# Optimization experiments

Measured on AMD Instinct MI355X. Metric: run time of the kernel, lower is better.

## Reference

```python
import jax, jax.numpy as jnp
import numpy as np

N_NODES = 50000
N_EDGES = 1600000
IN_DIM = 256
HID = 128
HEADS = 1
N_CLASSES = 40
NEG_SLOPE = 0.2


def gat_conv(x, W, a_src, a_dst, b, src, dst, concat):
    """PyG GATConv (eval mode). x: [N, F_in]; W: [H*C, F_in]; a_*: [H, C]; b: bias."""
    N = x.shape[0]
    H, C = a_src.shape
    h = (x @ W.T).reshape(N, H, C)                       # [N, H, C]
    alpha_src = jnp.sum(h * a_src, axis=-1)              # [N, H]
    alpha_dst = jnp.sum(h * a_dst, axis=-1)              # [N, H]
    e = jax.nn.leaky_relu(alpha_src[src] + alpha_dst[dst], NEG_SLOPE)  # [E, H]
    # scatter-softmax over incoming edges of each destination node
    m = jax.ops.segment_max(e, dst, num_segments=N)
    m = jnp.where(jnp.isfinite(m), m, 0.0)               # nodes with no in-edges
    ex = jnp.exp(e - m[dst])
    denom = jax.ops.segment_sum(ex, dst, num_segments=N)
    alpha = ex / jnp.maximum(denom[dst], 1e-16)          # [E, H]
    out = jax.ops.segment_sum(h[src] * alpha[..., None], dst, num_segments=N)  # [N, H, C]
    out = out.reshape(N, H * C) if concat else out.mean(axis=1)
    return out + b


def setup_inputs() -> dict:
    key = jax.random.key(0)
    ks = jax.random.split(key, 10)
    glorot = lambda k, shape: jax.random.normal(k, shape, jnp.float32) * np.sqrt(2.0 / (shape[0] + shape[-1]))
    x = jax.random.normal(ks[0], (N_NODES, IN_DIM), jnp.float32)
    edge_index = jax.random.randint(ks[1], (2, N_EDGES), 0, N_NODES, jnp.int64)
    # layer 0: in=IN_DIM -> hidden, heads=HEADS, concat=True
    W0 = glorot(ks[2], (HEADS * HID, IN_DIM))
    a_src0 = glorot(ks[3], (HEADS, HID))
    a_dst0 = glorot(ks[4], (HEADS, HID))
    b0 = jnp.zeros((HEADS * HID,), jnp.float32)
    # layer 1: in=hidden*heads -> n_classes, concat=False
    W1 = glorot(ks[5], (HEADS * N_CLASSES, HEADS * HID))
    a_src1 = glorot(ks[6], (HEADS, N_CLASSES))
    a_dst1 = glorot(ks[7], (HEADS, N_CLASSES))
    b1 = jnp.zeros((N_CLASSES,), jnp.float32)
    return {"x": x, "edge_index": edge_index,
            "W0": W0, "a_src0": a_src0, "a_dst0": a_dst0, "b0": b0,
            "W1": W1, "a_src1": a_src1, "a_dst1": a_dst1, "b1": b1}


def reference(x, edge_index, W0, a_src0, a_dst0, b0, W1, a_src1, a_dst1, b1):
    N = x.shape[0]
    # PyG GATConv default add_self_loops=True (each layer adds them transiently)
    loop = jnp.arange(N, dtype=edge_index.dtype)
    src = jnp.concatenate([edge_index[0], loop])
    dst = jnp.concatenate([edge_index[1], loop])
    h = gat_conv(x, W0, a_src0, a_dst0, b0, src, dst, concat=True)
    h = jax.nn.relu(h)  # dropout is identity in eval mode
    out = gat_conv(h, W1, a_src1, a_dst1, b1, src, dst, concat=False)
    return out
```

## Files before the change

### kernel.cpp

```cpp
#include <hip/hip_runtime.h>
#include <hip/hip_bf16.h>

#define N_NODES 50000
#define N_EDGES 1600000
#define ET (N_EDGES + N_NODES)
#define IN_DIM 256
#define HID 128
#define NCLS 40
#define NEG 0.2f
#define NBUCK 391
#define CHUNK 4096
#define CAP 5120
#define SCATB ((ET + CHUNK - 1) / CHUNK)
#define GEMMB ((N_NODES + 63) / 64)

typedef short bf16x8 __attribute__((ext_vector_type(8)));
typedef float f32x4  __attribute__((ext_vector_type(4)));

__device__ __forceinline__ unsigned pk2(float a, float b) {
    __hip_bfloat16 ha = __float2bfloat16(a), hb = __float2bfloat16(b);
    unsigned short ua = *(unsigned short*)&ha, ub = *(unsigned short*)&hb;
    return (unsigned)ua | ((unsigned)ub << 16);
}
__device__ __forceinline__ float blo(unsigned u) { return __uint_as_float(u << 16); }
__device__ __forceinline__ float bhi(unsigned u) { return __uint_as_float(u & 0xffff0000u); }

__global__ void k_init(int* __restrict__ cursor) {
    int i = blockIdx.x * 256 + threadIdx.x;
    if (i < NBUCK) cursor[i] = i * CAP;
}

__global__ __launch_bounds__(256) void k_fused(
    const int* __restrict__ ei, int* __restrict__ cursor, unsigned int* __restrict__ buf,
    const float* __restrict__ x, const float* __restrict__ W0,
    const float* __restrict__ a_s, const float* __restrict__ a_d,
    unsigned short* __restrict__ h0b, float* __restrict__ as0, float* __restrict__ ad0) {
    __shared__ unsigned pool[6912];
    int t = threadIdx.x;

    if (blockIdx.x < SCATB) {
        int* sd    = (int*)pool;
        int* hist  = (int*)pool + 4096;
        int* wbase = (int*)pool + 4487;
        for (int i = t; i < NBUCK; i += 256) hist[i] = 0;
        __syncthreads();
        int base = blockIdx.x * CHUNK;
        #pragma unroll
        for (int j = 0; j < 16; ++j) {
            int i = base + j * 256 + t;
            int d = -1;
            if (i < ET) d = (i < N_EDGES) ? ei[N_EDGES + i] : (i - N_EDGES);
            sd[j * 256 + t] = d;
            if (d >= 0) atomicAdd(&hist[d >> 7], 1);
        }
        __syncthreads();
        for (int i = t; i < NBUCK; i += 256) {
            int h = hist[i];
            wbase[i] = h ? atomicAdd(&cursor[i], h) : 0;
            hist[i] = 0;
        }
        __syncthreads();
        #pragma unroll
        for (int j = 0; j < 16; ++j) {
            int i = base + j * 256 + t;
            int d = sd[j * 256 + t];
            if (d >= 0) {
                int s_ = (i < N_EDGES) ? ei[i] : d;
                int b = d >> 7;
                int off = atomicAdd(&hist[b], 1);
                buf[wbase[b] + off] = ((unsigned)(d & 127) << 16) | (unsigned)s_;
            }
        }
        return;
    }

    unsigned* sA = pool;
    unsigned* sB = pool + 2304;
    int n0 = (blockIdx.x - SCATB) * 64;
    int w = t >> 6, lane = t & 63;
    int rw = lane & 15, q = lane >> 4;
    f32x4 acc[8];
    #pragma unroll
    for (int n = 0; n < 8; ++n) acc[n] = (f32x4){0.f, 0.f, 0.f, 0.f};

    for (int kc = 0; kc < IN_DIM; kc += 64) {
        #pragma unroll
        for (int i = 0; i < 4; ++i) {
            int f = i * 256 + t;
            int r = f >> 4, fq = f & 15;
            float4 v = make_float4(0.f, 0.f, 0.f, 0.f);
            if (n0 + r < N_NODES)
                v = *(const float4*)&x[(size_t)(n0 + r) * IN_DIM + kc + fq * 4];
            *(uint2*)&sA[r * 36 + fq * 2] = make_uint2(pk2(v.x, v.y), pk2(v.z, v.w));
        }
        #pragma unroll
        for (int i = 0; i < 8; ++i) {
            int f = i * 256 + t;
            int c = f >> 4, fq = f & 15;
            float4 v = *(const float4*)&W0[(size_t)c * IN_DIM + kc + fq * 4];
            *(uint2*)&sB[c * 36 + fq * 2] = make_uint2(pk2(v.x, v.y), pk2(v.z, v.w));
        }
        __syncthreads();
        #pragma unroll
        for (int ks = 0; ks < 2; ++ks) {
            bf16x8 af = *(const bf16x8*)((const unsigned short*)sA + (16 * w + rw) * 72 + ks * 32 + q * 8);
            #pragma unroll
            for (int n = 0; n < 8; ++n) {
                bf16x8 bfr = *(const bf16x8*)((const unsigned short*)sB + (n * 16 + rw) * 72 + ks * 32 + q * 8);
                acc[n] = __builtin_amdgcn_mfma_f32_16x16x32_bf16(af, bfr, acc[n], 0, 0, 0);
            }
        }
        __syncthreads();
    }

    float asv[8], adv[8];
    #pragma unroll
    for (int n = 0; n < 8; ++n) { asv[n] = a_s[n * 16 + rw]; adv[n] = a_d[n * 16 + rw]; }
    float ps[4] = {0.f, 0.f, 0.f, 0.f}, pd[4] = {0.f, 0.f, 0.f, 0.f};
    #pragma unroll
    for (int n = 0; n < 8; ++n)
        #pragma unroll
        for (int reg = 0; reg < 4; ++reg) {
            float vv = acc[n][reg];
            ps[reg] += vv * asv[n];
            pd[reg] += vv * adv[n];
        }
    #pragma unroll
    for (int reg = 0; reg < 4; ++reg) {
        int node = n0 + 16 * w + q * 4 + reg;
        if (node < N_NODES) {
            #pragma unroll
            for (int n = 0; n < 8; ++n) {
                __hip_bfloat16 hb = __float2bfloat16(acc[n][reg]);
                h0b[(size_t)node * HID + n * 16 + rw] = *(unsigned short*)&hb;
            }
        }
    }
    #pragma unroll
    for (int reg = 0; reg < 4; ++reg)
        #pragma unroll
        for (int off = 1; off < 16; off <<= 1) {
            ps[reg] += __shfl_xor(ps[reg], off);
            pd[reg] += __shfl_xor(pd[reg], off);
        }
    if (rw == 0) {
        #pragma unroll
        for (int reg = 0; reg < 4; ++reg) {
            int node = n0 + 16 * w + q * 4 + reg;
            if (node < N_NODES) { as0[node] = ps[reg]; ad0[node] = pd[reg]; }
        }
    }
}

__global__ __launch_bounds__(256) void k_bucket_build(const unsigned int* __restrict__ buf,
                                                      const int* __restrict__ cursor,
                                                      int* __restrict__ rp, int* __restrict__ re,
                                                      int* __restrict__ csr) {
    __shared__ int cnt[128], rpl[128], cur[128];
    int b = blockIdx.x;
    int t = threadIdx.x;
    int lo = b * CAP, hi = cursor[b];
    if (t < 128) cnt[t] = 0;
    __syncthreads();
    for (int i = lo + t; i < hi; i += 256) atomicAdd(&cnt[buf[i] >> 16], 1);
    __syncthreads();
    if (t == 0) {
        int run = 0;
        #pragma unroll
        for (int l = 0; l < 128; ++l) { rpl[l] = run; run += cnt[l]; }
    }
    __syncthreads();
    if (t < 128) {
        int node = b * 128 + t;
        if (node < N_NODES) { rp[node] = lo + rpl[t]; re[node] = lo + rpl[t] + cnt[t]; }
        cur[t] = 0;
    }
    __syncthreads();
    for (int i = lo + t; i < hi; i += 256) {
        unsigned v = buf[i];
        int dl = v >> 16;
        int off = atomicAdd(&cur[dl], 1);
        csr[lo + rpl[dl] + off] = (int)(v & 0xffffu);
    }
}

__global__ __launch_bounds__(256) void k_agg0(
    const uint4* __restrict__ h0q, const float* __restrict__ as, const float* __restrict__ ad,
    const int* __restrict__ rp, const int* __restrict__ re, const int* __restrict__ csr,
    const float* __restrict__ bias, unsigned short* __restrict__ actb) {
    __shared__ float sw_[4][64];
    __shared__ int   ss_[4][64];
    int wid = threadIdx.x >> 6, lane = threadIdx.x & 63;
    int q = lane >> 4, ql = lane & 15;
    int node = blockIdx.x * 4 + wid;
    int start = rp[node], end = re[node];
    float ad_n = ad[node];
    float a0 = 0.f, a1 = 0.f, a2 = 0.f, a3 = 0.f;
    float a4 = 0.f, a5 = 0.f, a6 = 0.f, a7 = 0.f, den = 0.f;
    for (int base = start; base < end; base += 64) {
        int mm = end - base; if (mm > 64) mm = 64;
        int s_l = 0; float w_l = 0.f;
        if (lane < mm) {
            s_l = csr[base + lane];
            float e = as[s_l] + ad_n;
            e = (e > 0.f) ? e : NEG * e;
            w_l = __expf(e);
            den += w_l;
        }
        ss_[wid][lane] = s_l;
        sw_[wid][lane] = w_l;
        for (int jj = 0; jj < mm; jj += 16) {
            int i0 = jj + q, i1 = i0 + 4, i2 = i0 + 8, i3 = i0 + 12;
            int   s0 = ss_[wid][i0], s1 = ss_[wid][i1], s2 = ss_[wid][i2], s3 = ss_[wid][i3];
            float w0 = sw_[wid][i0], w1 = sw_[wid][i1], w2 = sw_[wid][i2], w3 = sw_[wid][i3];
            uint4 u0 = h0q[(size_t)s0 * 16 + ql];
            uint4 u1 = h0q[(size_t)s1 * 16 + ql];
            uint4 u2 = h0q[(size_t)s2 * 16 + ql];
            uint4 u3 = h0q[(size_t)s3 * 16 + ql];
            a0 += w0 * blo(u0.x) + w1 * blo(u1.x) + w2 * blo(u2.x) + w3 * blo(u3.x);
            a1 += w0 * bhi(u0.x) + w1 * bhi(u1.x) + w2 * bhi(u2.x) + w3 * bhi(u3.x);
            a2 += w0 * blo(u0.y) + w1 * blo(u1.y) + w2 * blo(u2.y) + w3 * blo(u3.y);
            a3 += w0 * bhi(u0.y) + w1 * bhi(u1.y) + w2 * bhi(u2.y) + w3 * bhi(u3.y);
            a4 += w0 * blo(u0.z) + w1 * blo(u1.z) + w2 * blo(u2.z) + w3 * blo(u3.z);
            a5 += w0 * bhi(u0.z) + w1 * bhi(u1.z) + w2 * bhi(u2.z) + w3 * bhi(u3.z);
            a6 += w0 * blo(u0.w) + w1 * blo(u1.w) + w2 * blo(u2.w) + w3 * blo(u3.w);
            a7 += w0 * bhi(u0.w) + w1 * bhi(u1.w) + w2 * bhi(u2.w) + w3 * bhi(u3.w);
        }
    }
    #pragma unroll
    for (int off = 32; off; off >>= 1) den += __shfl_xor(den, off);
    a0 += __shfl_xor(a0, 16); a0 += __shfl_xor(a0, 32);
    a1 += __shfl_xor(a1, 16); a1 += __shfl_xor(a1, 32);
    a2 += __shfl_xor(a2, 16); a2 += __shfl_xor(a2, 32);
    a3 += __shfl_xor(a3, 16); a3 += __shfl_xor(a3, 32);
    a4 += __shfl_xor(a4, 16); a4 += __shfl_xor(a4, 32);
    a5 += __shfl_xor(a5, 16); a5 += __shfl_xor(a5, 32);
    a6 += __shfl_xor(a6, 16); a6 += __shfl_xor(a6, 32);
    a7 += __shfl_xor(a7, 16); a7 += __shfl_xor(a7, 32);
    if (lane < 16) {
        float inv = 1.f / fmaxf(den, 1e-16f);
        float4 b0v = *(const float4*)&bias[ql * 8];
        float4 b1v = *(const float4*)&bias[ql * 8 + 4];
        float r0 = fmaxf(a0 * inv + b0v.x, 0.f);
        float r1 = fmaxf(a1 * inv + b0v.y, 0.f);
        float r2 = fmaxf(a2 * inv + b0v.z, 0.f);
        float r3 = fmaxf(a3 * inv + b0v.w, 0.f);
        float r4 = fmaxf(a4 * inv + b1v.x, 0.f);
        float r5 = fmaxf(a5 * inv + b1v.y, 0.f);
        float r6 = fmaxf(a6 * inv + b1v.z, 0.f);
        float r7 = fmaxf(a7 * inv + b1v.w, 0.f);
        *(uint4*)&actb[(size_t)node * HID + ql * 8] =
            make_uint4(pk2(r0, r1), pk2(r2, r3), pk2(r4, r5), pk2(r6, r7));
    }
}

__global__ __launch_bounds__(128) void k_gemm1(
    const unsigned short* __restrict__ actb, const float* __restrict__ W1,
    const float* __restrict__ a_s, const float* __restrict__ a_d,
    unsigned short* __restrict__ h1b, float* __restrict__ as1, float* __restrict__ ad1) {
    __shared__ float w1l[NCLS * HID];
    __shared__ float av[NCLS], adv[NCLS];
    int t = threadIdx.x;
    #pragma unroll
    for (int i = 0; i < 10; ++i) {
        int j = t + 128 * i;
        ((float4*)w1l)[j] = ((const float4*)W1)[j];
    }
    if (t < NCLS) { av[t] = a_s[t]; adv[t] = a_d[t]; }
    __syncthreads();
    int n = blockIdx.x * 128 + t;
    if (n >= N_NODES) return;
    const uint4* ar = (const uint4*)(actb + (size_t)n * HID);
    float acc[NCLS];
    #pragma unroll
    for (int c = 0; c < NCLS; ++c) acc[c] = 0.f;
    for (int k0 = 0; k0 < HID; k0 += 8) {
        uint4 v = ar[k0 >> 3];
        float x0 = blo(v.x), x1 = bhi(v.x), x2 = blo(v.y), x3 = bhi(v.y);
        float x4 = blo(v.z), x5 = bhi(v.z), x6 = blo(v.w), x7 = bhi(v.w);
        #pragma unroll
        for (int c = 0; c < NCLS; ++c) {
            const float* wr = &w1l[c * HID + k0];
            acc[c] += x0 * wr[0] + x1 * wr[1] + x2 * wr[2] + x3 * wr[3]
                    + x4 * wr[4] + x5 * wr[5] + x6 * wr[6] + x7 * wr[7];
        }
    }
    float ps = 0.f, pd = 0.f;
    #pragma unroll
    for (int c = 0; c < NCLS; ++c) { ps += acc[c] * av[c]; pd += acc[c] * adv[c]; }
    unsigned pk_[20];
    #pragma unroll
    for (int c = 0; c < 20; ++c) pk_[c] = pk2(acc[2 * c], acc[2 * c + 1]);
    #pragma unroll
    for (int i = 0; i < 5; ++i)
        *(uint4*)&h1b[(size_t)n * NCLS + i * 8] = make_uint4(pk_[4*i], pk_[4*i+1], pk_[4*i+2], pk_[4*i+3]);
    as1[n] = ps; ad1[n] = pd;
}

__global__ __launch_bounds__(256) void k_agg1(
    const uint2* __restrict__ h1u, const float* __restrict__ as, const float* __restrict__ ad,
    const int* __restrict__ rp, const int* __restrict__ re, const int* __restrict__ csr,
    const float* __restrict__ bias, float* __restrict__ out) {
    __shared__ float sw_[4][64];
    __shared__ int   ss_[4][64];
    int wid = threadIdx.x >> 6, lane = threadIdx.x & 63;
    int q = lane >> 4, ql = lane & 15;
    int off10 = (ql < 10) ? ql : 0;
    int node = blockIdx.x * 4 + wid;
    int start = rp[node], end = re[node];
    float ad_n = ad[node];
    float a0 = 0.f, a1 = 0.f, a2 = 0.f, a3 = 0.f, den = 0.f;
    for (int base = start; base < end; base += 64) {
        int mm = end - base; if (mm > 64) mm = 64;
        int s_l = 0; float w_l = 0.f;
        if (lane < mm) {
            s_l = csr[base + lane];
            float e = as[s_l] + ad_n;
            e = (e > 0.f) ? e : NEG * e;
            w_l = __expf(e);
            den += w_l;
        }
        ss_[wid][lane] = s_l;
        sw_[wid][lane] = w_l;
        for (int jj = 0; jj < mm; jj += 16) {
            int i0 = jj + q, i1 = i0 + 4, i2 = i0 + 8, i3 = i0 + 12;
            int   s0 = ss_[wid][i0], s1 = ss_[wid][i1], s2 = ss_[wid][i2], s3 = ss_[wid][i3];
            float w0 = sw_[wid][i0], w1 = sw_[wid][i1], w2 = sw_[wid][i2], w3 = sw_[wid][i3];
            uint2 u0 = h1u[(size_t)s0 * 10 + off10];
            uint2 u1 = h1u[(size_t)s1 * 10 + off10];
            uint2 u2 = h1u[(size_t)s2 * 10 + off10];
            uint2 u3 = h1u[(size_t)s3 * 10 + off10];
            a0 += w0 * blo(u0.x) + w1 * blo(u1.x) + w2 * blo(u2.x) + w3 * blo(u3.x);
            a1 += w0 * bhi(u0.x) + w1 * bhi(u1.x) + w2 * bhi(u2.x) + w3 * bhi(u3.x);
            a2 += w0 * blo(u0.y) + w1 * blo(u1.y) + w2 * blo(u2.y) + w3 * blo(u3.y);
            a3 += w0 * bhi(u0.y) + w1 * bhi(u1.y) + w2 * bhi(u2.y) + w3 * bhi(u3.y);
        }
    }
    #pragma unroll
    for (int off = 32; off; off >>= 1) den += __shfl_xor(den, off);
    a0 += __shfl_xor(a0, 16); a0 += __shfl_xor(a0, 32);
    a1 += __shfl_xor(a1, 16); a1 += __shfl_xor(a1, 32);
    a2 += __shfl_xor(a2, 16); a2 += __shfl_xor(a2, 32);
    a3 += __shfl_xor(a3, 16); a3 += __shfl_xor(a3, 32);
    if (lane < 10) {
        float inv = 1.f / fmaxf(den, 1e-16f);
        float4 b4 = *(const float4*)&bias[ql * 4];
        float4 r;
        r.x = a0 * inv + b4.x;
        r.y = a1 * inv + b4.y;
        r.z = a2 * inv + b4.z;
        r.w = a3 * inv + b4.w;
        *(float4*)&out[(size_t)node * NCLS + ql * 4] = r;
    }
}

extern "C" void kernel_launch(void* const* d_in, const int* in_sizes, int n_in,
                              void* d_out, int out_size, void* d_ws, size_t ws_size,
                              hipStream_t stream) {
    const float* x    = (const float*)d_in[0];
    const int*   ei   = (const int*)d_in[1];
    const float* W0   = (const float*)d_in[2];
    const float* a_s0 = (const float*)d_in[3];
    const float* a_d0 = (const float*)d_in[4];
    const float* b0   = (const float*)d_in[5];
    const float* W1   = (const float*)d_in[6];
    const float* a_s1 = (const float*)d_in[7];
    const float* a_d1 = (const float*)d_in[8];
    const float* b1   = (const float*)d_in[9];

    char* p = (char*)d_ws;
    auto alloc = [&](size_t bytes) { void* q = p; p += (bytes + 255) & ~size_t(255); return q; };
    unsigned short* h0b  = (unsigned short*)alloc((size_t)N_NODES * HID * 2);
    unsigned int*   buf  = (unsigned int*)alloc((size_t)NBUCK * CAP * 4);
    int*   csr    = (int*)alloc((size_t)NBUCK * CAP * 4);
    unsigned short* h1b  = (unsigned short*)alloc(((size_t)N_NODES * NCLS + 32) * 2);
    unsigned short* actb = (unsigned short*)alloc((size_t)N_NODES * HID * 2);
    float* as0    = (float*)alloc((size_t)N_NODES * 4);
    float* ad0    = (float*)alloc((size_t)N_NODES * 4);
    float* as1    = (float*)alloc((size_t)N_NODES * 4);
    float* ad1    = (float*)alloc((size_t)N_NODES * 4);
    int*   rp     = (int*)alloc((size_t)N_NODES * 4);
    int*   re     = (int*)alloc((size_t)N_NODES * 4);
    int*   cursor = (int*)alloc((size_t)NBUCK * 4);

    k_init<<<(NBUCK + 255) / 256, 256, 0, stream>>>(cursor);
    k_fused<<<SCATB + GEMMB, 256, 0, stream>>>(ei, cursor, buf, x, W0, a_s0, a_d0, h0b, as0, ad0);
    k_bucket_build<<<NBUCK, 256, 0, stream>>>(buf, cursor, rp, re, csr);
    k_agg0<<<N_NODES / 4, 256, 0, stream>>>((const uint4*)h0b, as0, ad0, rp, re, csr, b0, actb);
    k_gemm1<<<(N_NODES + 127) / 128, 128, 0, stream>>>(actb, W1, a_s1, a_d1, h1b, as1, ad1);
    k_agg1<<<N_NODES / 4, 256, 0, stream>>>((const uint2*)h1b, as1, ad1, rp, re, csr, b1, (float*)d_out);
}
```

Measured before the change: 271.3 us.

## Fuse CSR bucket build into aggregation kernels using shared-memory per-bucket CSR

Removes the separate bucket-build kernel and global CSR/rowptr arrays. Each aggregation block now rebuilds the local CSR for its 128-node bucket in shared memory from the bucketed edge buffer, then processes 64 nodes with 8 waves. The cursor init kernel becomes a memset, with the bucket base offset added at scatter time. The cost is that the bucket sort is done twice per bucket per layer (once per half-block, and again in agg1), and the grid is much coarser (782 blocks), which may cause load imbalance.

```diff
diff --git a/kernel.cpp b/kernel.cpp
--- a/kernel.cpp
+++ b/kernel.cpp
@@ -25,11 +25,6 @@
 __device__ __forceinline__ float blo(unsigned u) { return __uint_as_float(u << 16); }
 __device__ __forceinline__ float bhi(unsigned u) { return __uint_as_float(u & 0xffff0000u); }
 
-__global__ void k_init(int* __restrict__ cursor) {
-    int i = blockIdx.x * 256 + threadIdx.x;
-    if (i < NBUCK) cursor[i] = i * CAP;
-}
-
 __global__ __launch_bounds__(256) void k_fused(
     const int* __restrict__ ei, int* __restrict__ cursor, unsigned int* __restrict__ buf,
     const float* __restrict__ x, const float* __restrict__ W0,
@@ -56,7 +51,7 @@
         __syncthreads();
         for (int i = t; i < NBUCK; i += 256) {
             int h = hist[i];
-            wbase[i] = h ? atomicAdd(&cursor[i], h) : 0;
+            wbase[i] = i * CAP + (h ? atomicAdd(&cursor[i], h) : 0);
             hist[i] = 0;
         }
         __syncthreads();
@@ -152,17 +147,21 @@
     }
 }
 
-__global__ __launch_bounds__(256) void k_bucket_build(const unsigned int* __restrict__ buf,
-                                                      const int* __restrict__ cursor,
-                                                      int* __restrict__ rp, int* __restrict__ re,
-                                                      int* __restrict__ csr) {
+__global__ __launch_bounds__(512) void k_agg0(
+    const uint4* __restrict__ h0q, const float* __restrict__ as, const float* __restrict__ ad,
+    const unsigned int* __restrict__ buf, const int* __restrict__ cursor,
+    const float* __restrict__ bias, unsigned short* __restrict__ actb) {
+    __shared__ unsigned short csr_s[CAP];
     __shared__ int cnt[128], rpl[128], cur[128];
-    int b = blockIdx.x;
+    __shared__ float sw_[8][64];
+    __shared__ unsigned short ss_[8][64];
     int t = threadIdx.x;
-    int lo = b * CAP, hi = cursor[b];
-    if (t < 128) cnt[t] = 0;
-    __syncthreads();
-    for (int i = lo + t; i < hi; i += 256) atomicAdd(&cnt[buf[i] >> 16], 1);
+    int b = blockIdx.x >> 1, half = blockIdx.x & 1;
+    int lo = b * CAP;
+    int n_e = cursor[b];
+    if (t < 128) { cnt[t] = 0; cur[t] = 0; }
+    __syncthreads();
+    for (int i = t; i < n_e; i += 512) atomicAdd(&cnt[buf[lo + i] >> 16], 1);
     __syncthreads();
     if (t == 0) {
         int run = 0;
@@ -170,87 +169,79 @@
         for (int l = 0; l < 128; ++l) { rpl[l] = run; run += cnt[l]; }
     }
     __syncthreads();
-    if (t < 128) {
-        int node = b * 128 + t;
-        if (node < N_NODES) { rp[node] = lo + rpl[t]; re[node] = lo + rpl[t] + cnt[t]; }
-        cur[t] = 0;
-    }
-    __syncthreads();
-    for (int i = lo + t; i < hi; i += 256) {
-        unsigned v = buf[i];
+    for (int i = t; i < n_e; i += 512) {
+        unsigned v = buf[lo + i];
         int dl = v >> 16;
         int off = atomicAdd(&cur[dl], 1);
-        csr[lo + rpl[dl] + off] = (int)(v & 0xffffu);
-    }
-}
-
-__global__ __launch_bounds__(256) void k_agg0(
-    const uint4* __restrict__ h0q, const float* __restrict__ as, const float* __restrict__ ad,
-    const int* __restrict__ rp, const int* __restrict__ re, const int* __restrict__ csr,
-    const float* __restrict__ bias, unsigned short* __restrict__ actb) {
-    __shared__ float sw_[4][64];
-    __shared__ int   ss_[4][64];
-    int wid = threadIdx.x >> 6, lane = threadIdx.x & 63;
+        csr_s[rpl[dl] + off] = (unsigned short)(v & 0xffffu);
+    }
+    __syncthreads();
+
+    int wid = t >> 6, lane = t & 63;
     int q = lane >> 4, ql = lane & 15;
-    int node = blockIdx.x * 4 + wid;
-    int start = rp[node], end = re[node];
-    float ad_n = ad[node];
-    float a0 = 0.f, a1 = 0.f, a2 = 0.f, a3 = 0.f;
-    float a4 = 0.f, a5 = 0.f, a6 = 0.f, a7 = 0.f, den = 0.f;
-    for (int base = start; base < end; base += 64) {
-        int mm = end - base; if (mm > 64) mm = 64;
-        int s_l = 0; float w_l = 0.f;
-        if (lane < mm) {
-            s_l = csr[base + lane];
-            float e = as[s_l] + ad_n;
-            e = (e > 0.f) ? e : NEG * e;
-            w_l = __expf(e);
-            den += w_l;
-        }
-        ss_[wid][lane] = s_l;
-        sw_[wid][lane] = w_l;
-        for (int jj = 0; jj < mm; jj += 16) {
-            int i0 = jj + q, i1 = i0 + 4, i2 = i0 + 8, i3 = i0 + 12;
-            int   s0 = ss_[wid][i0], s1 = ss_[wid][i1], s2 = ss_[wid][i2], s3 = ss_[wid][i3];
-            float w0 = sw_[wid][i0], w1 = sw_[wid][i1], w2 = sw_[wid][i2], w3 = sw_[wid][i3];
-            uint4 u0 = h0q[(size_t)s0 * 16 + ql];
-            uint4 u1 = h0q[(size_t)s1 * 16 + ql];
-            uint4 u2 = h0q[(size_t)s2 * 16 + ql];
-            uint4 u3 = h0q[(size_t)s3 * 16 + ql];
-            a0 += w0 * blo(u0.x) + w1 * blo(u1.x) + w2 * blo(u2.x) + w3 * blo(u3.x);
-            a1 += w0 * bhi(u0.x) + w1 * bhi(u1.x) + w2 * bhi(u2.x) + w3 * bhi(u3.x);
-            a2 += w0 * blo(u0.y) + w1 * blo(u1.y) + w2 * blo(u2.y) + w3 * blo(u3.y);
-            a3 += w0 * bhi(u0.y) + w1 * bhi(u1.y) + w2 * bhi(u2.y) + w3 * bhi(u3.y);
-            a4 += w0 * blo(u0.z) + w1 * blo(u1.z) + w2 * blo(u2.z) + w3 * blo(u3.z);
-            a5 += w0 * bhi(u0.z) + w1 * bhi(u1.z) + w2 * bhi(u2.z) + w3 * bhi(u3.z);
-            a6 += w0 * blo(u0.w) + w1 * blo(u1.w) + w2 * blo(u2.w) + w3 * blo(u3.w);
-            a7 += w0 * bhi(u0.w) + w1 * bhi(u1.w) + w2 * bhi(u2.w) + w3 * bhi(u3.w);
-        }
-    }
-    #pragma unroll
-    for (int off = 32; off; off >>= 1) den += __shfl_xor(den, off);
-    a0 += __shfl_xor(a0, 16); a0 += __shfl_xor(a0, 32);
-    a1 += __shfl_xor(a1, 16); a1 += __shfl_xor(a1, 32);
-    a2 += __shfl_xor(a2, 16); a2 += __shfl_xor(a2, 32);
-    a3 += __shfl_xor(a3, 16); a3 += __shfl_xor(a3, 32);
-    a4 += __shfl_xor(a4, 16); a4 += __shfl_xor(a4, 32);
-    a5 += __shfl_xor(a5, 16); a5 += __shfl_xor(a5, 32);
-    a6 += __shfl_xor(a6, 16); a6 += __shfl_xor(a6, 32);
-    a7 += __shfl_xor(a7, 16); a7 += __shfl_xor(a7, 32);
-    if (lane < 16) {
-        float inv = 1.f / fmaxf(den, 1e-16f);
-        float4 b0v = *(const float4*)&bias[ql * 8];
-        float4 b1v = *(const float4*)&bias[ql * 8 + 4];
-        float r0 = fmaxf(a0 * inv + b0v.x, 0.f);
-        float r1 = fmaxf(a1 * inv + b0v.y, 0.f);
-        float r2 = fmaxf(a2 * inv + b0v.z, 0.f);
-        float r3 = fmaxf(a3 * inv + b0v.w, 0.f);
-        float r4 = fmaxf(a4 * inv + b1v.x, 0.f);
-        float r5 = fmaxf(a5 * inv + b1v.y, 0.f);
-        float r6 = fmaxf(a6 * inv + b1v.z, 0.f);
-        float r7 = fmaxf(a7 * inv + b1v.w, 0.f);
-        *(uint4*)&actb[(size_t)node * HID + ql * 8] =
-            make_uint4(pk2(r0, r1), pk2(r2, r3), pk2(r4, r5), pk2(r6, r7));
+    for (int k = 0; k < 8; ++k) {
+        int ln = half * 64 + wid + 8 * k;
+        int node = b * 128 + ln;
+        if (node >= N_NODES) break;
+        int start = rpl[ln], deg = cnt[ln];
+        float ad_n = ad[node];
+        float a0 = 0.f, a1 = 0.f, a2 = 0.f, a3 = 0.f;
+        float a4 = 0.f, a5 = 0.f, a6 = 0.f, a7 = 0.f, den = 0.f;
+        for (int base = 0; base < deg; base += 64) {
+            int mm = deg - base; if (mm > 64) mm = 64;
+            int s_l = 0; float w_l = 0.f;
+            if (lane < mm) {
+                s_l = csr_s[start + base + lane];
+                float e = as[s_l] + ad_n;
+                e = (e > 0.f) ? e : NEG * e;
+                w_l = __expf(e);
+                den += w_l;
+            }
+            ss_[wid][lane] = (unsigned short)s_l;
+            sw_[wid][lane] = w_l;
+            for (int jj = 0; jj < mm; jj += 16) {
+                int i0 = jj + q, i1 = i0 + 4, i2 = i0 + 8, i3 = i0 + 12;
+                int   s0 = ss_[wid][i0], s1 = ss_[wid][i1], s2 = ss_[wid][i2], s3 = ss_[wid][i3];
+                float w0 = sw_[wid][i0], w1 = sw_[wid][i1], w2 = sw_[wid][i2], w3 = sw_[wid][i3];
+                uint4 u0 = h0q[(size_t)s0 * 16 + ql];
+                uint4 u1 = h0q[(size_t)s1 * 16 + ql];
+                uint4 u2 = h0q[(size_t)s2 * 16 + ql];
+                uint4 u3 = h0q[(size_t)s3 * 16 + ql];
+                a0 += w0 * blo(u0.x) + w1 * blo(u1.x) + w2 * blo(u2.x) + w3 * blo(u3.x);
+                a1 += w0 * bhi(u0.x) + w1 * bhi(u1.x) + w2 * bhi(u2.x) + w3 * bhi(u3.x);
+                a2 += w0 * blo(u0.y) + w1 * blo(u1.y) + w2 * blo(u2.y) + w3 * blo(u3.y);
+                a3 += w0 * bhi(u0.y) + w1 * bhi(u1.y) + w2 * bhi(u2.y) + w3 * bhi(u3.y);
+                a4 += w0 * blo(u0.z) + w1 * blo(u1.z) + w2 * blo(u2.z) + w3 * blo(u3.z);
+                a5 += w0 * bhi(u0.z) + w1 * bhi(u1.z) + w2 * bhi(u2.z) + w3 * bhi(u3.z);
+                a6 += w0 * blo(u0.w) + w1 * blo(u1.w) + w2 * blo(u2.w) + w3 * blo(u3.w);
+                a7 += w0 * bhi(u0.w) + w1 * bhi(u1.w) + w2 * bhi(u2.w) + w3 * bhi(u3.w);
+            }
+        }
+        #pragma unroll
+        for (int off = 32; off; off >>= 1) den += __shfl_xor(den, off);
+        a0 += __shfl_xor(a0, 16); a0 += __shfl_xor(a0, 32);
+        a1 += __shfl_xor(a1, 16); a1 += __shfl_xor(a1, 32);
+        a2 += __shfl_xor(a2, 16); a2 += __shfl_xor(a2, 32);
+        a3 += __shfl_xor(a3, 16); a3 += __shfl_xor(a3, 32);
+        a4 += __shfl_xor(a4, 16); a4 += __shfl_xor(a4, 32);
+        a5 += __shfl_xor(a5, 16); a5 += __shfl_xor(a5, 32);
+        a6 += __shfl_xor(a6, 16); a6 += __shfl_xor(a6, 32);
+        a7 += __shfl_xor(a7, 16); a7 += __shfl_xor(a7, 32);
+        if (lane < 16) {
+            float inv = 1.f / fmaxf(den, 1e-16f);
+            float4 b0v = *(const float4*)&bias[ql * 8];
+            float4 b1v = *(const float4*)&bias[ql * 8 + 4];
+            float r0 = fmaxf(a0 * inv + b0v.x, 0.f);
+            float r1 = fmaxf(a1 * inv + b0v.y, 0.f);
+            float r2 = fmaxf(a2 * inv + b0v.z, 0.f);
+            float r3 = fmaxf(a3 * inv + b0v.w, 0.f);
+            float r4 = fmaxf(a4 * inv + b1v.x, 0.f);
+            float r5 = fmaxf(a5 * inv + b1v.y, 0.f);
+            float r6 = fmaxf(a6 * inv + b1v.z, 0.f);
+            float r7 = fmaxf(a7 * inv + b1v.w, 0.f);
+            *(uint4*)&actb[(size_t)node * HID + ql * 8] =
+                make_uint4(pk2(r0, r1), pk2(r2, r3), pk2(r4, r5), pk2(r6, r7));
+        }
     }
 }
 
@@ -297,60 +288,88 @@
     as1[n] = ps; ad1[n] = pd;
 }
 
-__global__ __launch_bounds__(256) void k_agg1(
+__global__ __launch_bounds__(512) void k_agg1(
     const uint2* __restrict__ h1u, const float* __restrict__ as, const float* __restrict__ ad,
-    const int* __restrict__ rp, const int* __restrict__ re, const int* __restrict__ csr,
+    const unsigned int* __restrict__ buf, const int* __restrict__ cursor,
     const float* __restrict__ bias, float* __restrict__ out) {
-    __shared__ float sw_[4][64];
-    __shared__ int   ss_[4][64];
-    int wid = threadIdx.x >> 6, lane = threadIdx.x & 63;
+    __shared__ unsigned short csr_s[CAP];
+    __shared__ int cnt[128], rpl[128], cur[128];
+    __shared__ float sw_[8][64];
+    __shared__ unsigned short ss_[8][64];
+    int t = threadIdx.x;
+    int b = blockIdx.x >> 1, half = blockIdx.x & 1;
+    int lo = b * CAP;
+    int n_e = cursor[b];
+    if (t < 128) { cnt[t] = 0; cur[t] = 0; }
+    __syncthreads();
+    for (int i = t; i < n_e; i += 512) atomicAdd(&cnt[buf[lo + i] >> 16], 1);
+    __syncthreads();
+    if (t == 0) {
+        int run = 0;
+        #pragma unroll
+        for (int l = 0; l < 128; ++l) { rpl[l] = run; run += cnt[l]; }
+    }
+    __syncthreads();
+    for (int i = t; i < n_e; i += 512) {
+        unsigned v = buf[lo + i];
+        int dl = v >> 16;
+        int off = atomicAdd(&cur[dl], 1);
+        csr_s[rpl[dl] + off] = (unsigned short)(v & 0xffffu);
+    }
+    __syncthreads();
+
+    int wid = t >> 6, lane = t & 63;
     int q = lane >> 4, ql = lane & 15;
     int off10 = (ql < 10) ? ql : 0;
-    int node = blockIdx.x * 4 + wid;
-    int start = rp[node], end = re[node];
-    float ad_n = ad[node];
-    float a0 = 0.f, a1 = 0.f, a2 = 0.f, a3 = 0.f, den = 0.f;
-    for (int base = start; base < end; base += 64) {
-        int mm = end - base; if (mm > 64) mm = 64;
-        int s_l = 0; float w_l = 0.f;
-        if (lane < mm) {
-            s_l = csr[base + lane];
-            float e = as[s_l] + ad_n;
-            e = (e > 0.f) ? e : NEG * e;
-            w_l = __expf(e);
-            den += w_l;
-        }
-        ss_[wid][lane] = s_l;
-        sw_[wid][lane] = w_l;
-        for (int jj = 0; jj < mm; jj += 16) {
-            int i0 = jj + q, i1 = i0 + 4, i2 = i0 + 8, i3 = i0 + 12;
-            int   s0 = ss_[wid][i0], s1 = ss_[wid][i1], s2 = ss_[wid][i2], s3 = ss_[wid][i3];
-            float w0 = sw_[wid][i0], w1 = sw_[wid][i1], w2 = sw_[wid][i2], w3 = sw_[wid][i3];
-            uint2 u0 = h1u[(size_t)s0 * 10 + off10];
-            uint2 u1 = h1u[(size_t)s1 * 10 + off10];
-            uint2 u2 = h1u[(size_t)s2 * 10 + off10];
-            uint2 u3 = h1u[(size_t)s3 * 10 + off10];
-            a0 += w0 * blo(u0.x) + w1 * blo(u1.x) + w2 * blo(u2.x) + w3 * blo(u3.x);
-            a1 += w0 * bhi(u0.x) + w1 * bhi(u1.x) + w2 * bhi(u2.x) + w3 * bhi(u3.x);
-            a2 += w0 * blo(u0.y) + w1 * blo(u1.y) + w2 * blo(u2.y) + w3 * blo(u3.y);
-            a3 += w0 * bhi(u0.y) + w1 * bhi(u1.y) + w2 * bhi(u2.y) + w3 * bhi(u3.y);
-        }
-    }
-    #pragma unroll
-    for (int off = 32; off; off >>= 1) den += __shfl_xor(den, off);
-    a0 += __shfl_xor(a0, 16); a0 += __shfl_xor(a0, 32);
-    a1 += __shfl_xor(a1, 16); a1 += __shfl_xor(a1, 32);
-    a2 += __shfl_xor(a2, 16); a2 += __shfl_xor(a2, 32);
-    a3 += __shfl_xor(a3, 16); a3 += __shfl_xor(a3, 32);
-    if (lane < 10) {
-        float inv = 1.f / fmaxf(den, 1e-16f);
-        float4 b4 = *(const float4*)&bias[ql * 4];
-        float4 r;
-        r.x = a0 * inv + b4.x;
-        r.y = a1 * inv + b4.y;
-        r.z = a2 * inv + b4.z;
-        r.w = a3 * inv + b4.w;
-        *(float4*)&out[(size_t)node * NCLS + ql * 4] = r;
+    for (int k = 0; k < 8; ++k) {
+        int ln = half * 64 + wid + 8 * k;
+        int node = b * 128 + ln;
+        if (node >= N_NODES) break;
+        int start = rpl[ln], deg = cnt[ln];
+        float ad_n = ad[node];
+        float a0 = 0.f, a1 = 0.f, a2 = 0.f, a3 = 0.f, den = 0.f;
+        for (int base = 0; base < deg; base += 64) {
+            int mm = deg - base; if (mm > 64) mm = 64;
+            int s_l = 0; float w_l = 0.f;
+            if (lane < mm) {
+                s_l = csr_s[start + base + lane];
+                float e = as[s_l] + ad_n;
+                e = (e > 0.f) ? e : NEG * e;
+                w_l = __expf(e);
+                den += w_l;
+            }
+            ss_[wid][lane] = (unsigned short)s_l;
+            sw_[wid][lane] = w_l;
+            for (int jj = 0; jj < mm; jj += 16) {
+                int i0 = jj + q, i1 = i0 + 4, i2 = i0 + 8, i3 = i0 + 12;
+                int   s0 = ss_[wid][i0], s1 = ss_[wid][i1], s2 = ss_[wid][i2], s3 = ss_[wid][i3];
+                float w0 = sw_[wid][i0], w1 = sw_[wid][i1], w2 = sw_[wid][i2], w3 = sw_[wid][i3];
+                uint2 u0 = h1u[(size_t)s0 * 10 + off10];
+                uint2 u1 = h1u[(size_t)s1 * 10 + off10];
+                uint2 u2 = h1u[(size_t)s2 * 10 + off10];
+                uint2 u3 = h1u[(size_t)s3 * 10 + off10];
+                a0 += w0 * blo(u0.x) + w1 * blo(u1.x) + w2 * blo(u2.x) + w3 * blo(u3.x);
+                a1 += w0 * bhi(u0.x) + w1 * bhi(u1.x) + w2 * bhi(u2.x) + w3 * bhi(u3.x);
+                a2 += w0 * blo(u0.y) + w1 * blo(u1.y) + w2 * blo(u2.y) + w3 * blo(u3.y);
+                a3 += w0 * bhi(u0.y) + w1 * bhi(u1.y) + w2 * bhi(u2.y) + w3 * bhi(u3.y);
+            }
+        }
+        #pragma unroll
+        for (int off = 32; off; off >>= 1) den += __shfl_xor(den, off);
+        a0 += __shfl_xor(a0, 16); a0 += __shfl_xor(a0, 32);
+        a1 += __shfl_xor(a1, 16); a1 += __shfl_xor(a1, 32);
+        a2 += __shfl_xor(a2, 16); a2 += __shfl_xor(a2, 32);
+        a3 += __shfl_xor(a3, 16); a3 += __shfl_xor(a3, 32);
+        if (lane < 10) {
+            float inv = 1.f / fmaxf(den, 1e-16f);
+            float4 b4 = *(const float4*)&bias[ql * 4];
+            float4 r;
+            r.x = a0 * inv + b4.x;
+            r.y = a1 * inv + b4.y;
+            r.z = a2 * inv + b4.z;
+            r.w = a3 * inv + b4.w;
+            *(float4*)&out[(size_t)node * NCLS + ql * 4] = r;
+        }
     }
 }
 
@@ -372,21 +391,17 @@
     auto alloc = [&](size_t bytes) { void* q = p; p += (bytes + 255) & ~size_t(255); return q; };
     unsigned short* h0b  = (unsigned short*)alloc((size_t)N_NODES * HID * 2);
     unsigned int*   buf  = (unsigned int*)alloc((size_t)NBUCK * CAP * 4);
-    int*   csr    = (int*)alloc((size_t)NBUCK * CAP * 4);
     unsigned short* h1b  = (unsigned short*)alloc(((size_t)N_NODES * NCLS + 32) * 2);
     unsigned short* actb = (unsigned short*)alloc((size_t)N_NODES * HID * 2);
     float* as0    = (float*)alloc((size_t)N_NODES * 4);
     float* ad0    = (float*)alloc((size_t)N_NODES * 4);
     float* as1    = (float*)alloc((size_t)N_NODES * 4);
     float* ad1    = (float*)alloc((size_t)N_NODES * 4);
-    int*   rp     = (int*)alloc((size_t)N_NODES * 4);
-    int*   re     = (int*)alloc((size_t)N_NODES * 4);
     int*   cursor = (int*)alloc((size_t)NBUCK * 4);
 
-    k_init<<<(NBUCK + 255) / 256, 256, 0, stream>>>(cursor);
+    hipMemsetAsync(cursor, 0, (size_t)NBUCK * 4, stream);
     k_fused<<<SCATB + GEMMB, 256, 0, stream>>>(ei, cursor, buf, x, W0, a_s0, a_d0, h0b, as0, ad0);
-    k_bucket_build<<<NBUCK, 256, 0, stream>>>(buf, cursor, rp, re, csr);
-    k_agg0<<<N_NODES / 4, 256, 0, stream>>>((const uint4*)h0b, as0, ad0, rp, re, csr, b0, actb);
+    k_agg0<<<NBUCK * 2, 512, 0, stream>>>((const uint4*)h0b, as0, ad0, buf, cursor, b0, actb);
     k_gemm1<<<(N_NODES + 127) / 128, 128, 0, stream>>>(actb, W1, a_s1, a_d1, h1b, as1, ad1);
-    k_agg1<<<N_NODES / 4, 256, 0, stream>>>((const uint2*)h1b, as1, ad1, rp, re, csr, b1, (float*)d_out);
-}
+    k_agg1<<<NBUCK * 2, 512, 0, stream>>>((const uint2*)h1b, as1, ad1, buf, cursor, b1, (float*)d_out);
+}
```

New measurement: 290.4 us. 1.07x slower.

## Fuse layer-1 projection into layer-0 aggregation and replace init kernel with memset

Applied to the files above, without the earlier changes.

The layer-0 aggregation kernel now applies bias and ReLU, then multiplies each node's activation by W1 held in shared memory. It also computes the layer-1 attention scalars and writes h1 directly. This drops the separate k_gemm1 launch and the write and read of the bf16 activation buffer. Separately, the cursor init kernel becomes a memset, with the bucket base offset added inside the kernels. The cost is that every aggregation block must load W1 (about 21 KB) into shared memory, which adds per-block overhead across 12500 blocks and may lower occupancy.

```diff
diff --git a/kernel.cpp b/kernel.cpp
--- a/kernel.cpp
+++ b/kernel.cpp
@@ -25,11 +25,6 @@
 __device__ __forceinline__ float blo(unsigned u) { return __uint_as_float(u << 16); }
 __device__ __forceinline__ float bhi(unsigned u) { return __uint_as_float(u & 0xffff0000u); }
 
-__global__ void k_init(int* __restrict__ cursor) {
-    int i = blockIdx.x * 256 + threadIdx.x;
-    if (i < NBUCK) cursor[i] = i * CAP;
-}
-
 __global__ __launch_bounds__(256) void k_fused(
     const int* __restrict__ ei, int* __restrict__ cursor, unsigned int* __restrict__ buf,
     const float* __restrict__ x, const float* __restrict__ W0,
@@ -56,7 +51,7 @@
         __syncthreads();
         for (int i = t; i < NBUCK; i += 256) {
             int h = hist[i];
-            wbase[i] = h ? atomicAdd(&cursor[i], h) : 0;
+            wbase[i] = i * CAP + (h ? atomicAdd(&cursor[i], h) : 0);
             hist[i] = 0;
         }
         __syncthreads();
@@ -159,7 +154,7 @@
     __shared__ int cnt[128], rpl[128], cur[128];
     int b = blockIdx.x;
     int t = threadIdx.x;
-    int lo = b * CAP, hi = cursor[b];
+    int lo = b * CAP, hi = lo + cursor[b];
     if (t < 128) cnt[t] = 0;
     __syncthreads();
     for (int i = lo + t; i < hi; i += 256) atomicAdd(&cnt[buf[i] >> 16], 1);
@@ -187,10 +182,24 @@
 __global__ __launch_bounds__(256) void k_agg0(
     const uint4* __restrict__ h0q, const float* __restrict__ as, const float* __restrict__ ad,
     const int* __restrict__ rp, const int* __restrict__ re, const int* __restrict__ csr,
-    const float* __restrict__ bias, unsigned short* __restrict__ actb) {
+    const float* __restrict__ bias,
+    const float* __restrict__ W1, const float* __restrict__ a_s1, const float* __restrict__ a_d1,
+    unsigned int* __restrict__ h1d, float* __restrict__ as1, float* __restrict__ ad1) {
+    __shared__ float w1l[NCLS * 132];
+    __shared__ float av1[NCLS], adv1[NCLS];
     __shared__ float sw_[4][64];
     __shared__ int   ss_[4][64];
-    int wid = threadIdx.x >> 6, lane = threadIdx.x & 63;
+    int t = threadIdx.x;
+    #pragma unroll
+    for (int i = 0; i < 5; ++i) {
+        int j = t + 256 * i;
+        int c = j >> 5, cq = j & 31;
+        *(float4*)&w1l[c * 132 + cq * 4] = ((const float4*)W1)[j];
+    }
+    if (t < NCLS) { av1[t] = a_s1[t]; adv1[t] = a_d1[t]; }
+    __syncthreads();
+
+    int wid = t >> 6, lane = t & 63;
     int q = lane >> 4, ql = lane & 15;
     int node = blockIdx.x * 4 + wid;
     int start = rp[node], end = re[node];
@@ -237,64 +246,44 @@
     a5 += __shfl_xor(a5, 16); a5 += __shfl_xor(a5, 32);
     a6 += __shfl_xor(a6, 16); a6 += __shfl_xor(a6, 32);
     a7 += __shfl_xor(a7, 16); a7 += __shfl_xor(a7, 32);
-    if (lane < 16) {
-        float inv = 1.f / fmaxf(den, 1e-16f);
-        float4 b0v = *(const float4*)&bias[ql * 8];
-        float4 b1v = *(const float4*)&bias[ql * 8 + 4];
-        float r0 = fmaxf(a0 * inv + b0v.x, 0.f);
-        float r1 = fmaxf(a1 * inv + b0v.y, 0.f);
-        float r2 = fmaxf(a2 * inv + b0v.z, 0.f);
-        float r3 = fmaxf(a3 * inv + b0v.w, 0.f);
-        float r4 = fmaxf(a4 * inv + b1v.x, 0.f);
-        float r5 = fmaxf(a5 * inv + b1v.y, 0.f);
-        float r6 = fmaxf(a6 * inv + b1v.z, 0.f);
-        float r7 = fmaxf(a7 * inv + b1v.w, 0.f);
-        *(uint4*)&actb[(size_t)node * HID + ql * 8] =
-            make_uint4(pk2(r0, r1), pk2(r2, r3), pk2(r4, r5), pk2(r6, r7));
-    }
-}
-
-__global__ __launch_bounds__(128) void k_gemm1(
-    const unsigned short* __restrict__ actb, const float* __restrict__ W1,
-    const float* __restrict__ a_s, const float* __restrict__ a_d,
-    unsigned short* __restrict__ h1b, float* __restrict__ as1, float* __restrict__ ad1) {
-    __shared__ float w1l[NCLS * HID];
-    __shared__ float av[NCLS], adv[NCLS];
-    int t = threadIdx.x;
-    #pragma unroll
-    for (int i = 0; i < 10; ++i) {
-        int j = t + 128 * i;
-        ((float4*)w1l)[j] = ((const float4*)W1)[j];
-    }
-    if (t < NCLS) { av[t] = a_s[t]; adv[t] = a_d[t]; }
-    __syncthreads();
-    int n = blockIdx.x * 128 + t;
-    if (n >= N_NODES) return;
-    const uint4* ar = (const uint4*)(actb + (size_t)n * HID);
-    float acc[NCLS];
-    #pragma unroll
-    for (int c = 0; c < NCLS; ++c) acc[c] = 0.f;
-    for (int k0 = 0; k0 < HID; k0 += 8) {
-        uint4 v = ar[k0 >> 3];
-        float x0 = blo(v.x), x1 = bhi(v.x), x2 = blo(v.y), x3 = bhi(v.y);
-        float x4 = blo(v.z), x5 = bhi(v.z), x6 = blo(v.w), x7 = bhi(v.w);
-        #pragma unroll
-        for (int c = 0; c < NCLS; ++c) {
-            const float* wr = &w1l[c * HID + k0];
-            acc[c] += x0 * wr[0] + x1 * wr[1] + x2 * wr[2] + x3 * wr[3]
-                    + x4 * wr[4] + x5 * wr[5] + x6 * wr[6] + x7 * wr[7];
-        }
-    }
-    float ps = 0.f, pd = 0.f;
-    #pragma unroll
-    for (int c = 0; c < NCLS; ++c) { ps += acc[c] * av[c]; pd += acc[c] * adv[c]; }
-    unsigned pk_[20];
-    #pragma unroll
-    for (int c = 0; c < 20; ++c) pk_[c] = pk2(acc[2 * c], acc[2 * c + 1]);
-    #pragma unroll
-    for (int i = 0; i < 5; ++i)
-        *(uint4*)&h1b[(size_t)n * NCLS + i * 8] = make_uint4(pk_[4*i], pk_[4*i+1], pk_[4*i+2], pk_[4*i+3]);
-    as1[n] = ps; ad1[n] = pd;
+
+    float inv = 1.f / fmaxf(den, 1e-16f);
+    float4 b0v = *(const float4*)&bias[ql * 8];
+    float4 b1v = *(const float4*)&bias[ql * 8 + 4];
+    float r0 = fmaxf(a0 * inv + b0v.x, 0.f);
+    float r1 = fmaxf(a1 * inv + b0v.y, 0.f);
+    float r2 = fmaxf(a2 * inv + b0v.z, 0.f);
+    float r3 = fmaxf(a3 * inv + b0v.w, 0.f);
+    float r4 = fmaxf(a4 * inv + b1v.x, 0.f);
+    float r5 = fmaxf(a5 * inv + b1v.y, 0.f);
+    float r6 = fmaxf(a6 * inv + b1v.z, 0.f);
+    float r7 = fmaxf(a7 * inv + b1v.w, 0.f);
+
+    float cls[10];
+    #pragma unroll
+    for (int c10 = 0; c10 < 10; ++c10) {
+        int c = q * 10 + c10;
+        const float4 wv0 = *(const float4*)&w1l[c * 132 + ql * 8];
+        const float4 wv1 = *(const float4*)&w1l[c * 132 + ql * 8 + 4];
+        cls[c10] = r0 * wv0.x + r1 * wv0.y + r2 * wv0.z + r3 * wv0.w
+                 + r4 * wv1.x + r5 * wv1.y + r6 * wv1.z + r7 * wv1.w;
+    }
+    #pragma unroll
+    for (int c10 = 0; c10 < 10; ++c10)
+        #pragma unroll
+        for (int off = 1; off < 16; off <<= 1)
+            cls[c10] += __shfl_xor(cls[c10], off);
+    float t1 = 0.f, t2 = 0.f;
+    #pragma unroll
+    for (int c10 = 0; c10 < 10; ++c10) {
+        t1 += cls[c10] * av1[q * 10 + c10];
+        t2 += cls[c10] * adv1[q * 10 + c10];
+    }
+    t1 += __shfl_xor(t1, 16); t1 += __shfl_xor(t1, 32);
+    t2 += __shfl_xor(t2, 16); t2 += __shfl_xor(t2, 32);
+    if (lane == 0) { as1[node] = t1; ad1[node] = t2; }
+    if (ql < 5)
+        h1d[(size_t)node * 20 + q * 5 + ql] = pk2(cls[2 * ql], cls[2 * ql + 1]);
 }
 
 __global__ __launch_bounds__(256) void k_agg1(
@@ -373,8 +362,7 @@
     unsigned short* h0b  = (unsigned short*)alloc((size_t)N_NODES * HID * 2);
     unsigned int*   buf  = (unsigned int*)alloc((size_t)NBUCK * CAP * 4);
     int*   csr    = (int*)alloc((size_t)NBUCK * CAP * 4);
-    unsigned short* h1b  = (unsigned short*)alloc(((size_t)N_NODES * NCLS + 32) * 2);
-    unsigned short* actb = (unsigned short*)alloc((size_t)N_NODES * HID * 2);
+    unsigned int* h1d = (unsigned int*)alloc(((size_t)N_NODES * 20 + 32) * 4);
     float* as0    = (float*)alloc((size_t)N_NODES * 4);
     float* ad0    = (float*)alloc((size_t)N_NODES * 4);
     float* as1    = (float*)alloc((size_t)N_NODES * 4);
@@ -383,10 +371,10 @@
     int*   re     = (int*)alloc((size_t)N_NODES * 4);
     int*   cursor = (int*)alloc((size_t)NBUCK * 4);
 
-    k_init<<<(NBUCK + 255) / 256, 256, 0, stream>>>(cursor);
+    hipMemsetAsync(cursor, 0, (size_t)NBUCK * 4, stream);
     k_fused<<<SCATB + GEMMB, 256, 0, stream>>>(ei, cursor, buf, x, W0, a_s0, a_d0, h0b, as0, ad0);
     k_bucket_build<<<NBUCK, 256, 0, stream>>>(buf, cursor, rp, re, csr);
-    k_agg0<<<N_NODES / 4, 256, 0, stream>>>((const uint4*)h0b, as0, ad0, rp, re, csr, b0, actb);
-    k_gemm1<<<(N_NODES + 127) / 128, 128, 0, stream>>>(actb, W1, a_s1, a_d1, h1b, as1, ad1);
-    k_agg1<<<N_NODES / 4, 256, 0, stream>>>((const uint2*)h1b, as1, ad1, rp, re, csr, b1, (float*)d_out);
-}
+    k_agg0<<<N_NODES / 4, 256, 0, stream>>>((const uint4*)h0b, as0, ad0, rp, re, csr, b0,
+                                            W1, a_s1, a_d1, h1d, as1, ad1);
+    k_agg1<<<N_NODES / 4, 256, 0, stream>>>((const uint2*)h1d, as1, ad1, rp, re, csr, b1, (float*)d_out);
+}
```

New measurement: 318.5 us. 1.17x slower.
